# Kernel tuning notes

Measured on AMD Instinct MI355X. Metric: run time of the kernel, lower is better.

Reference implementation:

```python
import jax, jax.numpy as jnp
import numpy as np

B, N, DIM = 2, 2048, 1024
H, DH = 16, 64            # num query heads, head dim (single shared kv head)
CTX_N, CTX_DIM = 256, 1024

def setup_inputs() -> dict:
    key = jax.random.key(0)
    ks = jax.random.split(key, 8)
    s = lambda fan: 1.0 / np.sqrt(fan)
    return {
        'x': jax.random.normal(ks[0], (B, N, DIM), jnp.float32),
        'context': jax.random.normal(ks[1], (B, CTX_N, CTX_DIM), jnp.float32),
        'g1': jnp.ones((DIM,), jnp.float32),
        'Wq': jax.random.normal(ks[2], (DIM, H * DH), jnp.float32) * s(DIM),
        'Wkv': jax.random.normal(ks[3], (DIM, 2 * DH), jnp.float32) * s(DIM),
        'null_kv': jax.random.normal(ks[4], (2, DH), jnp.float32) * s(DH),
        'ctx_g': jnp.ones((CTX_DIM,), jnp.float32),
        'ctx_b': jnp.zeros((CTX_DIM,), jnp.float32),
        'Wc': jax.random.normal(ks[5], (CTX_DIM, 2 * DH), jnp.float32) * s(CTX_DIM),
        'bc': jnp.zeros((2 * DH,), jnp.float32),
        'Wout': jax.random.normal(ks[6], (H * DH, DIM), jnp.float32) * s(H * DH),
        'g2': jnp.ones((DIM,), jnp.float32),
    }

def _ln_g(t, g, eps):
    # custom LayerNorm: scale only, no bias, population variance
    m = jnp.mean(t, axis=-1, keepdims=True)
    v = jnp.var(t, axis=-1, keepdims=True)
    return (t - m) / jnp.sqrt(v + eps) * g

def reference(x, context, g1, Wq, Wkv, null_kv, ctx_g, ctx_b, Wc, bc, Wout, g2):
    b, n, _ = x.shape
    scale = DH ** -0.5
    h = _ln_g(x, g1, 1e-5)                              # [b,n,dim]
    q = (h @ Wq).reshape(b, n, H, DH).transpose(0, 2, 1, 3) * scale  # [b,H,n,d]
    k, v = jnp.split(h @ Wkv, 2, axis=-1)               # each [b,n,d] (single kv head)
    # null kv token
    nk = jnp.broadcast_to(null_kv[0], (b, 1, DH))
    nv = jnp.broadcast_to(null_kv[1], (b, 1, DH))
    k = jnp.concatenate((k, nk), axis=-2)
    v = jnp.concatenate((v, nv), axis=-2)
    # context kv tokens (standard flax LayerNorm: scale+bias, eps=1e-6)
    cm = jnp.mean(context, axis=-1, keepdims=True)
    cv_ = jnp.var(context, axis=-1, keepdims=True)
    ch = (context - cm) / jnp.sqrt(cv_ + 1e-6) * ctx_g + ctx_b
    ck, cvv = jnp.split(ch @ Wc + bc, 2, axis=-1)       # [b,ctx_n,d]
    k = jnp.concatenate((k, ck), axis=-2)               # [b,j,d]
    v = jnp.concatenate((v, cvv), axis=-2)
    sim = jnp.einsum('bhid,bjd->bhij', q, k)            # shared kv head broadcast
    attn = jax.nn.softmax(sim, axis=-1)
    out = jnp.einsum('bhij,bjd->bhid', attn, v)
    out = out.transpose(0, 2, 1, 3).reshape(b, n, H * DH)
    out = out @ Wout
    return _ln_g(out, g2, 1e-5)
```

## Files before the change

### kernel.cpp

```cpp
#include <hip/hip_runtime.h>

typedef __attribute__((ext_vector_type(4)))  float  f32x4;
typedef __attribute__((ext_vector_type(16))) float  f32x16;
typedef __attribute__((ext_vector_type(8)))  short  s16x8;

#define DEVI __device__ __forceinline__

constexpr int Bb   = 2;
constexpr int Nn   = 2048;
constexpr int Hh   = 16;
constexpr int DHc  = 64;
constexpr int CTXN = 256;
constexpr int Jv   = Nn + 1 + CTXN;
constexpr int JP   = 2432;
constexpr int QKVN = Hh*DHc + 2*DHc;

DEVI unsigned short f2bf(float f) {
    union { float f; unsigned u; } v; v.f = f;
    unsigned r = v.u + 0x7fffu + ((v.u >> 16) & 1u);
    return (unsigned short)(r >> 16);
}
DEVI float bf2f(unsigned short h) {
    union { unsigned u; float f; } v; v.u = ((unsigned)h) << 16;
    return v.f;
}
DEVI unsigned cvt_pk_bf(float lo, float hi) {
    unsigned r;
    asm("v_cvt_pk_bf16_f32 %0, %1, %2" : "=v"(r) : "v"(lo), "v"(hi));
    return r;
}
DEVI float exp2v(float x) {
    float r;
    asm("v_exp_f32 %0, %1" : "=v"(r) : "v"(x));
    return r;
}
DEVI void gl_lds16(const void* g, void* l) {
    __builtin_amdgcn_global_load_lds(
        (__attribute__((address_space(1))) void*)g,
        (__attribute__((address_space(3))) void*)l,
        16, 0, 0);
}

__global__ __launch_bounds__(256) void k_pre(const float* __restrict__ Wq,
                                             const float* __restrict__ Wkv,
                                             const float* __restrict__ Wc,
                                             const float* __restrict__ Wout,
                                             const float* __restrict__ x,
                                             const float* __restrict__ ctx,
                                             const float* __restrict__ g1,
                                             const float* __restrict__ cg,
                                             const float* __restrict__ cb,
                                             unsigned short* __restrict__ WqkvT,
                                             unsigned short* __restrict__ WcT,
                                             unsigned short* __restrict__ WoutT,
                                             unsigned short* __restrict__ h,
                                             unsigned short* __restrict__ ch,
                                             float qscale) {
    int bxg = blockIdx.x;
    if (bxg < 2304) {
        __shared__ float tile[32][33];
        int bx = bxg % 72, by = bxg / 72;
        const float* in; unsigned short* out; int C; float scale; int cb_;
        if (bx < 32)      { in = Wq;   out = WqkvT;               C = 1024; scale = qscale; cb_ = bx; }
        else if (bx < 36) { in = Wkv;  out = WqkvT + 1024 * 1024; C = 128;  scale = 1.0f;  cb_ = bx - 32; }
        else if (bx < 40) { in = Wc;   out = WcT;                 C = 128;  scale = 1.0f;  cb_ = bx - 36; }
        else              { in = Wout; out = WoutT;               C = 1024; scale = 1.0f;  cb_ = bx - 40; }
        int tx = threadIdx.x & 31, ty = threadIdx.x >> 5;
        int r0 = by * 32, c0 = cb_ * 32;
#pragma unroll
        for (int i = 0; i < 32; i += 8)
            tile[ty + i][tx] = in[(size_t)(r0 + ty + i) * C + c0 + tx];
        __syncthreads();
#pragma unroll
        for (int i = 0; i < 32; i += 8)
            out[(size_t)(c0 + ty + i) * 1024 + r0 + tx] = f2bf(tile[tx][ty + i] * scale);
    } else {
        int row = bxg - 2304, tid = threadIdx.x;
        bool isx = row < 4096;
        const float* rp = isx ? x + (size_t)row * 1024 : ctx + (size_t)(row - 4096) * 1024;
        const float* g  = isx ? g1 : cg;
        float eps = isx ? 1e-5f : 1e-6f;
        unsigned short* o = isx ? h + (size_t)row * 1024 : ch + (size_t)(row - 4096) * 1024;

        f32x4 v = *(const f32x4*)(rp + tid * 4);
        float s = v.x + v.y + v.z + v.w;
        float q = v.x * v.x + v.y * v.y + v.z * v.z + v.w * v.w;
#pragma unroll
        for (int m = 32; m; m >>= 1) { s += __shfl_down(s, m, 64); q += __shfl_down(q, m, 64); }
        __shared__ float ss[4], sq[4];
        int wid = tid >> 6, lane = tid & 63;
        if (lane == 0) { ss[wid] = s; sq[wid] = q; }
        __syncthreads();
        s = ss[0] + ss[1] + ss[2] + ss[3];
        q = sq[0] + sq[1] + sq[2] + sq[3];
        float mean = s * (1.0f / 1024.0f);
        float var  = q * (1.0f / 1024.0f) - mean * mean;
        float rstd = rsqrtf(var + eps);
        f32x4 gg = *(const f32x4*)(g + tid * 4);
        f32x4 r;
#pragma unroll
        for (int e = 0; e < 4; e++) r[e] = (v[e] - mean) * rstd * gg[e];
        if (!isx) {
            f32x4 bb = *(const f32x4*)(cb + tid * 4);
#pragma unroll
            for (int e = 0; e < 4; e++) r[e] += bb[e];
        }
        uint2 ov = make_uint2(cvt_pk_bf(r[0], r[1]), cvt_pk_bf(r[2], r[3]));
        *(uint2*)(o + tid * 4) = ov;
    }
}

__global__ __launch_bounds__(256) void k_ln_out(const unsigned short* __restrict__ in,
                                                const float* __restrict__ g,
                                                float* __restrict__ out) {
    int row = blockIdx.x, tid = threadIdx.x;
    const unsigned short* rp = in + (size_t)row * 1024;
    uint2 raw = *(const uint2*)(rp + tid * 4);
    f32x4 v;
    v.x = bf2f((unsigned short)(raw.x & 0xffff));
    v.y = bf2f((unsigned short)(raw.x >> 16));
    v.z = bf2f((unsigned short)(raw.y & 0xffff));
    v.w = bf2f((unsigned short)(raw.y >> 16));
    float s = v.x + v.y + v.z + v.w;
    float q = v.x * v.x + v.y * v.y + v.z * v.z + v.w * v.w;
#pragma unroll
    for (int m = 32; m; m >>= 1) { s += __shfl_down(s, m, 64); q += __shfl_down(q, m, 64); }
    __shared__ float ss[4], sq[4];
    int wid = tid >> 6, lane = tid & 63;
    if (lane == 0) { ss[wid] = s; sq[wid] = q; }
    __syncthreads();
    s = ss[0] + ss[1] + ss[2] + ss[3];
    q = sq[0] + sq[1] + sq[2] + sq[3];
    float mean = s * (1.0f / 1024.0f);
    float var  = q * (1.0f / 1024.0f) - mean * mean;
    float rstd = rsqrtf(var + 1e-5f);
    f32x4 gg = *(const f32x4*)(g + tid * 4);
    f32x4 r;
#pragma unroll
    for (int e = 0; e < 4; e++) r[e] = (v[e] - mean) * rstd * gg[e];
    *(f32x4*)(out + (size_t)row * 1024 + tid * 4) = r;
}

template<int OUT_BF16>
DEVI void gemm128(unsigned short* Al, unsigned short* Bl,
                  const unsigned short* __restrict__ A,
                  const unsigned short* __restrict__ BT,
                  void* __restrict__ C,
                  int M, int N, int K, int bn, int bm) {
    int tid = threadIdx.x;
    int wid = tid >> 6, lane = tid & 63;
    int wm = wid >> 1, wn = wid & 1;
    int lr = lane & 15, lg = lane >> 4;
    int r8 = lane >> 3;
    int sl = (lane & 7) ^ r8;

    const unsigned short* Ag = A  + (size_t)(bm * 128 + wid * 32 + r8) * K + sl * 8;
    const unsigned short* Bg = BT + (size_t)(bn * 128 + wid * 32 + r8) * K + sl * 8;

    f32x4 acc[4][4] = {};
    int nk = K >> 6;
#pragma unroll 1
    for (int s = 0; s < nk; ++s) {
        int k0 = s << 6;
        __syncthreads();
#pragma unroll
        for (int i = 0; i < 4; i++) {
            gl_lds16(Ag + (size_t)i * 8 * K + k0, Al + wid * 2048 + i * 512);
            gl_lds16(Bg + (size_t)i * 8 * K + k0, Bl + wid * 2048 + i * 512);
        }
        __syncthreads();
#pragma unroll
        for (int kk = 0; kk < 2; kk++) {
            int co = ((kk * 4 + lg) ^ (lr & 7)) * 8;
            s16x8 af[4], bf[4];
#pragma unroll
            for (int mi = 0; mi < 4; mi++)
                af[mi] = *(const s16x8*)&Al[(wm * 64 + mi * 16 + lr) * 64 + co];
#pragma unroll
            for (int ni = 0; ni < 4; ni++)
                bf[ni] = *(const s16x8*)&Bl[(wn * 64 + ni * 16 + lr) * 64 + co];
#pragma unroll
            for (int mi = 0; mi < 4; mi++)
#pragma unroll
                for (int ni = 0; ni < 4; ni++)
                    acc[mi][ni] = __builtin_amdgcn_mfma_f32_16x16x32_bf16(af[mi], bf[ni], acc[mi][ni], 0, 0, 0);
        }
    }
#pragma unroll
    for (int mi = 0; mi < 4; mi++)
#pragma unroll
        for (int r = 0; r < 4; r++) {
            int row = bm * 128 + wm * 64 + mi * 16 + lg * 4 + r;
#pragma unroll
            for (int ni = 0; ni < 4; ni++) {
                int col = bn * 128 + wn * 64 + ni * 16 + lr;
                float val = acc[mi][ni][r];
                if (OUT_BF16)
                    ((unsigned short*)C)[(size_t)row * N + col] = f2bf(val);
                else
                    ((float*)C)[(size_t)row * N + col] = val;
            }
        }
}

__global__ __launch_bounds__(256) void k_gemm_qkv(const unsigned short* __restrict__ h,
                                                  const unsigned short* __restrict__ WqkvT,
                                                  unsigned short* __restrict__ qkv,
                                                  const unsigned short* __restrict__ ch,
                                                  const unsigned short* __restrict__ WcT,
                                                  unsigned short* __restrict__ ckv) {
    __shared__ unsigned short SA[128 * 64];
    __shared__ unsigned short SB[128 * 64];
    int id = blockIdx.x;
    if (id < 288)
        gemm128<1>(SA, SB, h, WqkvT, qkv, 4096, 1152, 1024, id % 9, id / 9);
    else
        gemm128<1>(SA, SB, ch, WcT, ckv, 512, 128, 1024, 0, id - 288);
}

__global__ __launch_bounds__(256) void k_gemm_out(const unsigned short* __restrict__ aout,
                                                  const unsigned short* __restrict__ WoutT,
                                                  unsigned short* __restrict__ preout) {
    __shared__ unsigned short SA[128 * 64];
    __shared__ unsigned short SB[128 * 64];
    int id = blockIdx.x;
    gemm128<1>(SA, SB, aout, WoutT, preout, 4096, 1024, 1024, id % 8, id / 8);
}

__global__ __launch_bounds__(256) void k_assemble_kv(const unsigned short* __restrict__ qkv,
                                                     const unsigned short* __restrict__ ckv,
                                                     const float* __restrict__ nkv,
                                                     const float* __restrict__ bc,
                                                     unsigned short* __restrict__ Kb,
                                                     unsigned short* __restrict__ Vt) {
    int idx = blockIdx.x * 256 + threadIdx.x;
    int d = idx & 63;
    int j = (idx >> 6) % JP;
    int b = idx / (64 * JP);
    float kv, vv;
    if (j < Nn) {
        const unsigned short* r = qkv + (size_t)(b * Nn + j) * QKVN + Hh * DHc;
        kv = bf2f(r[d]); vv = bf2f(r[64 + d]);
    } else if (j == Nn) {
        kv = nkv[d]; vv = nkv[64 + d];
    } else if (j < Jv) {
        const unsigned short* r = ckv + (size_t)(b * CTXN + (j - Nn - 1)) * 128;
        kv = bf2f(r[d]) + bc[d]; vv = bf2f(r[64 + d]) + bc[64 + d];
    } else {
        kv = 0.0f; vv = 0.0f;
    }
    Kb[((size_t)b * JP + j) * 64 + d] = f2bf(kv);
    Vt[((size_t)b * 64 + d) * JP + j] = f2bf(vv);
}

__global__ __launch_bounds__(512) void k_attn(const unsigned short* __restrict__ qkv,
                                              const unsigned short* __restrict__ Kb,
                                              const unsigned short* __restrict__ Vt,
                                              unsigned short* __restrict__ aout) {
    __shared__ unsigned short KV[2][2][2][64 * 64];

    int bid = blockIdx.x;
    int qt = bid & 15, h = (bid >> 4) & 15, b = bid >> 8;
    int tid = threadIdx.x, wid = tid >> 6, lane = tid & 63;
    int tm = wid >> 2, tw = wid & 3;
    int l31 = lane & 31, hi = lane >> 5;
    int n0 = qt * 128 + tw * 32;
    int r8 = lane >> 3;
    int sl = (lane & 7) ^ r8;
    int x7 = l31 & 7;
    int jb = tm * 1216;

    s16x8 qf[4];
#pragma unroll
    for (int kk = 0; kk < 4; kk++)
        qf[kk] = *(const s16x8*)(qkv + (size_t)(b * Nn + n0 + l31) * QKVN + h * 64 + kk * 16 + hi * 8);

    f32x16 O0 = {}, O1 = {};
    float Lv = 0.0f;

    const unsigned short* Kg = Kb + ((size_t)b * JP + jb + tw * 16 + r8) * 64 + sl * 8;
    const unsigned short* Vg = Vt + ((size_t)b * 64 + tw * 16 + r8) * JP + jb + sl * 8;

    auto stage = [&](int t, int buf) {
#pragma unroll
        for (int i = 0; i < 2; i++) {
            gl_lds16(Kg + ((size_t)t * 64 + i * 8) * 64, &KV[tm][buf][0][tw * 1024 + i * 512]);
            gl_lds16(Vg + (size_t)i * 8 * JP + t * 64,   &KV[tm][buf][1][tw * 1024 + i * 512]);
        }
    };

    auto build_pf = [&](const f32x16& s, int w) -> s16x8 {
        unsigned c0 = cvt_pk_bf(s[8 * w + 0], s[8 * w + 1]);
        unsigned c1 = cvt_pk_bf(s[8 * w + 2], s[8 * w + 3]);
        unsigned c2 = cvt_pk_bf(s[8 * w + 4], s[8 * w + 5]);
        unsigned c3 = cvt_pk_bf(s[8 * w + 6], s[8 * w + 7]);
        asm("v_permlane32_swap_b32 %0, %1" : "+v"(c0), "+v"(c2));
        asm("v_permlane32_swap_b32 %0, %1" : "+v"(c1), "+v"(c3));
        union { unsigned u[4]; s16x8 v; } pu;
        pu.u[0] = c0; pu.u[1] = c1; pu.u[2] = c2; pu.u[3] = c3;
        return pu.v;
    };

    stage(0, 0);
    asm volatile("s_waitcnt vmcnt(0)" ::: "memory");
    asm volatile("s_barrier" ::: "memory");
    int cur = 0;
#pragma unroll 1
    for (int t = 0; t < 19; ++t) {
        if (t < 18) {
            stage(t + 1, cur ^ 1);
            asm volatile("s_waitcnt vmcnt(4)" ::: "memory");
        } else {
            asm volatile("s_waitcnt vmcnt(0)" ::: "memory");
        }
        asm volatile("s_barrier" ::: "memory");
        __builtin_amdgcn_sched_barrier(0);
        const unsigned short* Kl = &KV[tm][cur][0][0];
        const unsigned short* Vl = &KV[tm][cur][1][0];
        int j0 = jb + t * 64;

        f32x16 s0 = {}, s1 = {};
        __builtin_amdgcn_s_setprio(1);
#pragma unroll
        for (int kk = 0; kk < 4; kk++) {
            int co = ((kk * 2 + hi) ^ x7) * 8;
            s16x8 k0 = *(const s16x8*)&Kl[l31 * 64 + co];
            s16x8 k1 = *(const s16x8*)&Kl[(32 + l31) * 64 + co];
            s0 = __builtin_amdgcn_mfma_f32_32x32x16_bf16(k0, qf[kk], s0, 0, 0, 0);
            s1 = __builtin_amdgcn_mfma_f32_32x32x16_bf16(k1, qf[kk], s1, 0, 0, 0);
        }
        __builtin_amdgcn_s_setprio(0);
        if (j0 + 64 > Jv) {
#pragma unroll
            for (int r = 0; r < 16; r++) {
                int ja = j0 + (r & 3) + 8 * (r >> 2) + 4 * hi;
                if (ja >= Jv)      s0[r] = -1e30f;
                if (ja + 32 >= Jv) s1[r] = -1e30f;
            }
        }

        float sum = 0.0f;
#pragma unroll
        for (int r = 0; r < 16; r++) { s0[r] = exp2v(s0[r]); sum += s0[r]; }
#pragma unroll
        for (int r = 0; r < 16; r++) { s1[r] = exp2v(s1[r]); sum += s1[r]; }
        Lv += sum;

        __builtin_amdgcn_s_setprio(1);
#pragma unroll
        for (int ks = 0; ks < 4; ks++) {
            s16x8 pf = (ks < 2) ? build_pf(s0, ks & 1) : build_pf(s1, ks & 1);
            int co = ((ks * 2 + hi) ^ x7) * 8;
            s16x8 v0 = *(const s16x8*)&Vl[l31 * 64 + co];
            s16x8 v1 = *(const s16x8*)&Vl[(32 + l31) * 64 + co];
            O0 = __builtin_amdgcn_mfma_f32_32x32x16_bf16(v0, pf, O0, 0, 0, 0);
            O1 = __builtin_amdgcn_mfma_f32_32x32x16_bf16(v1, pf, O1, 0, 0, 0);
        }
        __builtin_amdgcn_s_setprio(0);
        __builtin_amdgcn_sched_barrier(0);
        asm volatile("s_barrier" ::: "memory");
        cur ^= 1;
    }

    Lv += __shfl_xor(Lv, 32, 64);

    float* Ob = (float*)&KV[0][0][0][0];
    float* Ml = Ob + 4 * 64 * 33;
    unsigned short* slabs = (unsigned short*)(Ml + 4 * 64);

    __syncthreads();
    if (tm == 1) {
        float* dst = Ob + ((size_t)tw * 64 + lane) * 33;
#pragma unroll
        for (int r = 0; r < 16; r++) { dst[r] = O0[r]; dst[16 + r] = O1[r]; }
        Ml[tw * 64 + lane] = Lv;
    }
    __syncthreads();
    if (tm == 0) {
        const float* src = Ob + ((size_t)tw * 64 + lane) * 33;
        float rl = 1.0f / (Lv + Ml[tw * 64 + lane]);

        unsigned short* slab = slabs + tw * 2304;
#pragma unroll
        for (int rq = 0; rq < 4; rq++) {
            uint2 w0 = make_uint2(
                cvt_pk_bf((O0[rq * 4 + 0] + src[rq * 4 + 0]) * rl,
                          (O0[rq * 4 + 1] + src[rq * 4 + 1]) * rl),
                cvt_pk_bf((O0[rq * 4 + 2] + src[rq * 4 + 2]) * rl,
                          (O0[rq * 4 + 3] + src[rq * 4 + 3]) * rl));
            *(uint2*)&slab[l31 * 72 + rq * 8 + hi * 4] = w0;
            uint2 w1 = make_uint2(
                cvt_pk_bf((O1[rq * 4 + 0] + src[16 + rq * 4 + 0]) * rl,
                          (O1[rq * 4 + 1] + src[16 + rq * 4 + 1]) * rl),
                cvt_pk_bf((O1[rq * 4 + 2] + src[16 + rq * 4 + 2]) * rl,
                          (O1[rq * 4 + 3] + src[16 + rq * 4 + 3]) * rl));
            *(uint2*)&slab[l31 * 72 + 32 + rq * 8 + hi * 4] = w1;
        }
        int q = lane >> 1, half = lane & 1;
        const s16x8* srcq = (const s16x8*)&slab[q * 72 + half * 32];
        s16x8 o0 = srcq[0], o1 = srcq[1], o2 = srcq[2], o3 = srcq[3];
        unsigned short* gdst = aout + (size_t)(b * Nn + n0 + q) * 1024 + h * 64 + half * 32;
        *(s16x8*)gdst = o0;
        *((s16x8*)gdst + 1) = o1;
        *((s16x8*)gdst + 2) = o2;
        *((s16x8*)gdst + 3) = o3;
    }
}

extern "C" void kernel_launch(void* const* d_in, const int* in_sizes, int n_in,
                              void* d_out, int out_size, void* d_ws, size_t ws_size,
                              hipStream_t stream) {
    const float* x    = (const float*)d_in[0];
    const float* ctx  = (const float*)d_in[1];
    const float* g1   = (const float*)d_in[2];
    const float* Wq   = (const float*)d_in[3];
    const float* Wkv  = (const float*)d_in[4];
    const float* nkv  = (const float*)d_in[5];
    const float* ctxg = (const float*)d_in[6];
    const float* ctxb = (const float*)d_in[7];
    const float* Wc   = (const float*)d_in[8];
    const float* bc   = (const float*)d_in[9];
    const float* Wout = (const float*)d_in[10];
    const float* g2   = (const float*)d_in[11];
    float* out = (float*)d_out;

    char* w = (char*)d_ws;
    unsigned short* h_    = (unsigned short*)w; w += (size_t)4096 * 1024 * 2;
    unsigned short* ch    = (unsigned short*)w; w += (size_t)512 * 1024 * 2;
    unsigned short* WqkvT = (unsigned short*)w; w += (size_t)1152 * 1024 * 2;
    unsigned short* WcT   = (unsigned short*)w; w += (size_t)128 * 1024 * 2;
    unsigned short* WoutT = (unsigned short*)w; w += (size_t)1024 * 1024 * 2;
    unsigned short* qkv   = (unsigned short*)w; w += (size_t)4096 * 1152 * 2;
    unsigned short* ckv   = (unsigned short*)w; w += (size_t)512 * 128 * 2;
    unsigned short* Kb    = (unsigned short*)w; w += (size_t)Bb * JP * 64 * 2;
    unsigned short* Vt    = (unsigned short*)w; w += (size_t)Bb * 64 * JP * 2;
    unsigned short* aout  = (unsigned short*)w; w += (size_t)4096 * 1024 * 2;

    const float qscale = 0.125f * 1.4426950408889634f;

    k_pre<<<6912, 256, 0, stream>>>(Wq, Wkv, Wc, Wout, x, ctx, g1, ctxg, ctxb,
                                    WqkvT, WcT, WoutT, h_, ch, qscale);

    k_gemm_qkv<<<292, 256, 0, stream>>>(h_, WqkvT, qkv, ch, WcT, ckv);

    k_assemble_kv<<<(Bb * JP * 64) / 256, 256, 0, stream>>>(qkv, ckv, nkv, bc, Kb, Vt);

    k_attn<<<Bb * Hh * (Nn / 128), 512, 0, stream>>>(qkv, Kb, Vt, aout);

    k_gemm_out<<<256, 256, 0, stream>>>(aout, WoutT, h_);
    k_ln_out<<<4096, 256, 0, stream>>>(h_, g2, out);
}
```

Measured before the change: 114.7 us.

## Fuse KV assembly into GEMM epilogues and triple-buffer GEMM K-loop

Removes the separate k_assemble_kv kernel. The QKV GEMM epilogue now writes K and transposed V directly into the padded attention buffers, the context GEMM adds its bias and writes the same way, and k_pre gains one extra block that fills the null token and zero padding. Separately, the shared GEMM mainloop becomes a 3-stage LDS pipeline that issues global_load_lds two tiles ahead and waits with explicit vmcnt counts, so loads overlap MFMA work. This saves a launch and one pass over the KV data, but it triples LDS use per block (96KB), which may lower occupancy, and the Vt epilogue stores are strided and uncoalesced.

```diff
diff --git a/kernel.cpp b/kernel.cpp
--- a/kernel.cpp
+++ b/kernel.cpp
@@ -50,11 +50,14 @@
                                              const float* __restrict__ g1,
                                              const float* __restrict__ cg,
                                              const float* __restrict__ cb,
+                                             const float* __restrict__ nkv,
                                              unsigned short* __restrict__ WqkvT,
                                              unsigned short* __restrict__ WcT,
                                              unsigned short* __restrict__ WoutT,
                                              unsigned short* __restrict__ h,
                                              unsigned short* __restrict__ ch,
+                                             unsigned short* __restrict__ Kb,
+                                             unsigned short* __restrict__ Vt,
                                              float qscale) {
     int bxg = blockIdx.x;
     if (bxg < 2304) {
@@ -74,7 +77,7 @@
 #pragma unroll
         for (int i = 0; i < 32; i += 8)
             out[(size_t)(c0 + ty + i) * 1024 + r0 + tx] = f2bf(tile[tx][ty + i] * scale);
-    } else {
+    } else if (bxg < 6912) {
         int row = bxg - 2304, tid = threadIdx.x;
         bool isx = row < 4096;
         const float* rp = isx ? x + (size_t)row * 1024 : ctx + (size_t)(row - 4096) * 1024;
@@ -107,6 +110,21 @@
         }
         uint2 ov = make_uint2(cvt_pk_bf(r[0], r[1]), cvt_pk_bf(r[2], r[3]));
         *(uint2*)(o + tid * 4) = ov;
+    } else {
+        int t = threadIdx.x;
+        if (t < 128) {
+            int b = t >> 6, d = t & 63;
+            Kb[((size_t)b * JP + Nn) * 64 + d] = f2bf(nkv[d]);
+            Vt[((size_t)b * 64 + d) * JP + Nn] = f2bf(nkv[64 + d]);
+        }
+        for (int idx = t; idx < 2 * (JP - Jv) * 64; idx += 256) {
+            int b = idx / ((JP - Jv) * 64);
+            int rem = idx % ((JP - Jv) * 64);
+            int j = Jv + rem / 64;
+            int d = rem % 64;
+            Kb[((size_t)b * JP + j) * 64 + d] = 0;
+            Vt[((size_t)b * 64 + d) * JP + j] = 0;
+        }
     }
 }
 
@@ -141,12 +159,15 @@
     *(f32x4*)(out + (size_t)row * 1024 + tid * 4) = r;
 }
 
-template<int OUT_BF16>
-DEVI void gemm128(unsigned short* Al, unsigned short* Bl,
+template<int MODE>
+DEVI void gemm128(unsigned short* SAb, unsigned short* SBb,
                   const unsigned short* __restrict__ A,
                   const unsigned short* __restrict__ BT,
-                  void* __restrict__ C,
-                  int M, int N, int K, int bn, int bm) {
+                  unsigned short* __restrict__ C,
+                  int M, int N, int K, int bn, int bm,
+                  unsigned short* __restrict__ Kb,
+                  unsigned short* __restrict__ Vt,
+                  const float* __restrict__ bias) {
     int tid = threadIdx.x;
     int wid = tid >> 6, lane = tid & 63;
     int wm = wid >> 1, wn = wid & 1;
@@ -157,18 +178,37 @@
     const unsigned short* Ag = A  + (size_t)(bm * 128 + wid * 32 + r8) * K + sl * 8;
     const unsigned short* Bg = BT + (size_t)(bn * 128 + wid * 32 + r8) * K + sl * 8;
 
+    auto stage = [&](int buf, int s) {
+        int k0 = s << 6;
+        unsigned short* SA = SAb + buf * (128 * 64);
+        unsigned short* SB = SBb + buf * (128 * 64);
+#pragma unroll
+        for (int i = 0; i < 4; i++) {
+            gl_lds16(Ag + (size_t)i * 8 * K + k0, SA + wid * 2048 + i * 512);
+            gl_lds16(Bg + (size_t)i * 8 * K + k0, SB + wid * 2048 + i * 512);
+        }
+    };
+
     f32x4 acc[4][4] = {};
     int nk = K >> 6;
+    stage(0, 0);
+    stage(1, 1);
+    int b0 = 0;
 #pragma unroll 1
     for (int s = 0; s < nk; ++s) {
-        int k0 = s << 6;
-        __syncthreads();
-#pragma unroll
-        for (int i = 0; i < 4; i++) {
-            gl_lds16(Ag + (size_t)i * 8 * K + k0, Al + wid * 2048 + i * 512);
-            gl_lds16(Bg + (size_t)i * 8 * K + k0, Bl + wid * 2048 + i * 512);
-        }
-        __syncthreads();
+        int b2 = b0 + 2; if (b2 >= 3) b2 -= 3;
+        if (s + 2 < nk) {
+            stage(b2, s + 2);
+            asm volatile("s_waitcnt vmcnt(16)" ::: "memory");
+        } else if (s + 1 < nk) {
+            asm volatile("s_waitcnt vmcnt(8)" ::: "memory");
+        } else {
+            asm volatile("s_waitcnt vmcnt(0)" ::: "memory");
+        }
+        __builtin_amdgcn_s_barrier();
+        __builtin_amdgcn_sched_barrier(0);
+        const unsigned short* Al = SAb + b0 * (128 * 64);
+        const unsigned short* Bl = SBb + b0 * (128 * 64);
 #pragma unroll
         for (int kk = 0; kk < 2; kk++) {
             int co = ((kk * 4 + lg) ^ (lr & 7)) * 8;
@@ -185,6 +225,9 @@
                 for (int ni = 0; ni < 4; ni++)
                     acc[mi][ni] = __builtin_amdgcn_mfma_f32_16x16x32_bf16(af[mi], bf[ni], acc[mi][ni], 0, 0, 0);
         }
+        __builtin_amdgcn_sched_barrier(0);
+        __builtin_amdgcn_s_barrier();
+        b0 = b0 + 1; if (b0 >= 3) b0 = 0;
     }
 #pragma unroll
     for (int mi = 0; mi < 4; mi++)
@@ -195,10 +238,22 @@
             for (int ni = 0; ni < 4; ni++) {
                 int col = bn * 128 + wn * 64 + ni * 16 + lr;
                 float val = acc[mi][ni][r];
-                if (OUT_BF16)
-                    ((unsigned short*)C)[(size_t)row * N + col] = f2bf(val);
-                else
-                    ((float*)C)[(size_t)row * N + col] = val;
+                if (MODE == 0) {
+                    C[(size_t)row * N + col] = f2bf(val);
+                } else if (MODE == 1) {
+                    if (bn < 8) {
+                        C[(size_t)row * N + col] = f2bf(val);
+                    } else {
+                        int b = row >> 11, j = row & 2047, c = col - 1024;
+                        if (c < 64) Kb[((size_t)b * JP + j) * 64 + c] = f2bf(val);
+                        else        Vt[((size_t)b * 64 + (c - 64)) * JP + j] = f2bf(val);
+                    }
+                } else {
+                    int b = row >> 8, j = 2049 + (row & 255);
+                    float v2 = val + bias[col];
+                    if (col < 64) Kb[((size_t)b * JP + j) * 64 + col] = f2bf(v2);
+                    else          Vt[((size_t)b * 64 + (col - 64)) * JP + j] = f2bf(v2);
+                }
             }
         }
 }
@@ -208,49 +263,26 @@
                                                   unsigned short* __restrict__ qkv,
                                                   const unsigned short* __restrict__ ch,
                                                   const unsigned short* __restrict__ WcT,
-                                                  unsigned short* __restrict__ ckv) {
-    __shared__ unsigned short SA[128 * 64];
-    __shared__ unsigned short SB[128 * 64];
+                                                  unsigned short* __restrict__ Kb,
+                                                  unsigned short* __restrict__ Vt,
+                                                  const float* __restrict__ bc) {
+    __shared__ unsigned short SA[3][128 * 64];
+    __shared__ unsigned short SB[3][128 * 64];
     int id = blockIdx.x;
     if (id < 288)
-        gemm128<1>(SA, SB, h, WqkvT, qkv, 4096, 1152, 1024, id % 9, id / 9);
+        gemm128<1>(&SA[0][0], &SB[0][0], h, WqkvT, qkv, 4096, 1152, 1024, id % 9, id / 9, Kb, Vt, nullptr);
     else
-        gemm128<1>(SA, SB, ch, WcT, ckv, 512, 128, 1024, 0, id - 288);
+        gemm128<2>(&SA[0][0], &SB[0][0], ch, WcT, nullptr, 512, 128, 1024, 0, id - 288, Kb, Vt, bc);
 }
 
 __global__ __launch_bounds__(256) void k_gemm_out(const unsigned short* __restrict__ aout,
                                                   const unsigned short* __restrict__ WoutT,
                                                   unsigned short* __restrict__ preout) {
-    __shared__ unsigned short SA[128 * 64];
-    __shared__ unsigned short SB[128 * 64];
+    __shared__ unsigned short SA[3][128 * 64];
+    __shared__ unsigned short SB[3][128 * 64];
     int id = blockIdx.x;
-    gemm128<1>(SA, SB, aout, WoutT, preout, 4096, 1024, 1024, id % 8, id / 8);
-}
-
-__global__ __launch_bounds__(256) void k_assemble_kv(const unsigned short* __restrict__ qkv,
-                                                     const unsigned short* __restrict__ ckv,
-                                                     const float* __restrict__ nkv,
-                                                     const float* __restrict__ bc,
-                                                     unsigned short* __restrict__ Kb,
-                                                     unsigned short* __restrict__ Vt) {
-    int idx = blockIdx.x * 256 + threadIdx.x;
-    int d = idx & 63;
-    int j = (idx >> 6) % JP;
-    int b = idx / (64 * JP);
-    float kv, vv;
-    if (j < Nn) {
-        const unsigned short* r = qkv + (size_t)(b * Nn + j) * QKVN + Hh * DHc;
-        kv = bf2f(r[d]); vv = bf2f(r[64 + d]);
-    } else if (j == Nn) {
-        kv = nkv[d]; vv = nkv[64 + d];
-    } else if (j < Jv) {
-        const unsigned short* r = ckv + (size_t)(b * CTXN + (j - Nn - 1)) * 128;
-        kv = bf2f(r[d]) + bc[d]; vv = bf2f(r[64 + d]) + bc[64 + d];
-    } else {
-        kv = 0.0f; vv = 0.0f;
-    }
-    Kb[((size_t)b * JP + j) * 64 + d] = f2bf(kv);
-    Vt[((size_t)b * 64 + d) * JP + j] = f2bf(vv);
+    gemm128<0>(&SA[0][0], &SB[0][0], aout, WoutT, preout, 4096, 1024, 1024, id % 8, id / 8,
+               nullptr, nullptr, nullptr);
 }
 
 __global__ __launch_bounds__(512) void k_attn(const unsigned short* __restrict__ qkv,
@@ -430,20 +462,17 @@
     unsigned short* WqkvT = (unsigned short*)w; w += (size_t)1152 * 1024 * 2;
     unsigned short* WcT   = (unsigned short*)w; w += (size_t)128 * 1024 * 2;
     unsigned short* WoutT = (unsigned short*)w; w += (size_t)1024 * 1024 * 2;
-    unsigned short* qkv   = (unsigned short*)w; w += (size_t)4096 * 1152 * 2;
-    unsigned short* ckv   = (unsigned short*)w; w += (size_t)512 * 128 * 2;
+    unsigned short* qkv   = (unsigned short*)w; w += (size_t)4096 * QKVN * 2;
     unsigned short* Kb    = (unsigned short*)w; w += (size_t)Bb * JP * 64 * 2;
     unsigned short* Vt    = (unsigned short*)w; w += (size_t)Bb * 64 * JP * 2;
     unsigned short* aout  = (unsigned short*)w; w += (size_t)4096 * 1024 * 2;
 
     const float qscale = 0.125f * 1.4426950408889634f;
 
-    k_pre<<<6912, 256, 0, stream>>>(Wq, Wkv, Wc, Wout, x, ctx, g1, ctxg, ctxb,
-                                    WqkvT, WcT, WoutT, h_, ch, qscale);
-
-    k_gemm_qkv<<<292, 256, 0, stream>>>(h_, WqkvT, qkv, ch, WcT, ckv);
-
-    k_assemble_kv<<<(Bb * JP * 64) / 256, 256, 0, stream>>>(qkv, ckv, nkv, bc, Kb, Vt);
+    k_pre<<<6913, 256, 0, stream>>>(Wq, Wkv, Wc, Wout, x, ctx, g1, ctxg, ctxb, nkv,
+                                    WqkvT, WcT, WoutT, h_, ch, Kb, Vt, qscale);
+
+    k_gemm_qkv<<<292, 256, 0, stream>>>(h_, WqkvT, qkv, ch, WcT, Kb, Vt, bc);
 
     k_attn<<<Bb * Hh * (Nn / 128), 512, 0, stream>>>(qkv, Kb, Vt, aout);
 
```

New measurement: 136.0 us. 1.19x slower.
